# Performance work log

Measured on AMD Instinct MI355X. Metric: run time of the kernel, lower is better.

Reference implementation:

```python
import jax, jax.numpy as jnp
import numpy as np

EPS = 1e-12  # torch F.normalize default eps

def _l2norm(x, axis=-1):
    n = jnp.linalg.norm(x, axis=axis, keepdims=True)
    return x / jnp.maximum(n, EPS)

def setup_inputs() -> dict:
    key = jax.random.key(0)
    k1, k2 = jax.random.split(key)
    query = jax.random.normal(k1, (65536, 512), dtype=jnp.float32)
    prototypes = jax.random.normal(k2, (64, 512), dtype=jnp.float32)
    return {"query": query, "prototypes": prototypes, "k": 3}

def reference(query, prototypes, k):
    # cosine similarity between queries and prototypes: [B, P]
    sim = jnp.einsum('bd,pd->bp', _l2norm(query), _l2norm(prototypes))
    k = min(int(k), prototypes.shape[0])
    weights, indices = jax.lax.top_k(sim, k)          # [B, k]
    retrieved = prototypes[indices]                   # [B, k, D]
    w = jax.nn.softmax(weights, axis=1)               # [B, k]
    return jnp.einsum('bkd,bk->bd', retrieved, w)     # [B, D]
```

## Files before the change

### kernel.cpp

```cpp
#include <hip/hip_runtime.h>
#include <math.h>

#define DIM 512
#define NP  64
#define TAU 4e-5f
#define LISTCAP 8192
#define RFB 128

#define WS_PTW   0
#define WS_BHI   131072
#define WS_BLO   196608
#define WS_INV64 262144
#define WS_CNT   262656
#define WS_LIST  262784

typedef __attribute__((ext_vector_type(8))) short bf16x8;
typedef __attribute__((ext_vector_type(8))) unsigned short u16x8;
typedef __attribute__((ext_vector_type(4))) float f32x4;

__device__ __forceinline__ unsigned short f2bf(float f) {
  const unsigned int u = __float_as_uint(f);
  return (unsigned short)((u + 0x7FFFu + ((u >> 16) & 1u)) >> 16);
}
__device__ __forceinline__ float bf2f(unsigned short h) {
  return __uint_as_float(((unsigned int)h) << 16);
}

__device__ __forceinline__ void gload_lds16(const void* g, void* l) {
  __builtin_amdgcn_global_load_lds(
      (const __attribute__((address_space(1))) void*)g,
      (__attribute__((address_space(3))) void*)l, 16, 0, 0);
}

__device__ __forceinline__ void ins4f(float v, int idx, float& v0, float& v1,
                                      float& v2, float& v3, int& j0, int& j1,
                                      int& j2, int& j3) {
  const bool b0 = v > v0, b1 = v > v1, b2 = v > v2, b3 = v > v3;
  v3 = b2 ? v2 : (b3 ? v : v3);  j3 = b2 ? j2 : (b3 ? idx : j3);
  v2 = b1 ? v1 : (b2 ? v : v2);  j2 = b1 ? j1 : (b2 ? idx : j2);
  v1 = b0 ? v0 : (b1 ? v : v1);  j1 = b0 ? j0 : (b1 ? idx : j1);
  v0 = b0 ? v  : v0;             j0 = b0 ? idx : j0;
}

__device__ __forceinline__ void ins3d(double v, int idx, double& b0, double& b1,
                                      double& b2, int& k0, int& k1, int& k2) {
  const bool c0 = v > b0, c1 = v > b1, c2 = v > b2;
  b2 = c1 ? b1 : (c2 ? v : b2);  k2 = c1 ? k1 : (c2 ? idx : k2);
  b1 = c0 ? b0 : (c1 ? v : b1);  k1 = c0 ? k0 : (c1 ? idx : k1);
  b0 = c0 ? v  : b0;             k0 = c0 ? idx : k0;
}

__global__ __launch_bounds__(256) void prep_all_kernel(
    const float* __restrict__ protos, float* __restrict__ ptw,
    unsigned short* __restrict__ bhi, unsigned short* __restrict__ blo,
    double* __restrict__ inv64, int* __restrict__ cnt) {
  if (blockIdx.x == 0 && threadIdx.x == 0) *cnt = 0;
  const int p = blockIdx.x * 4 + (threadIdx.x >> 6);
  const int lane = threadIdx.x & 63;
  const float4* pr = (const float4*)(protos + (size_t)p * DIM);
  const float4 a = pr[lane * 2];
  const float4 b = pr[lane * 2 + 1];
  double ss = (double)a.x * a.x + (double)a.y * a.y + (double)a.z * a.z +
              (double)a.w * a.w + (double)b.x * b.x + (double)b.y * b.y +
              (double)b.z * b.z + (double)b.w * b.w;
#pragma unroll
  for (int m = 1; m < 64; m <<= 1) ss += __shfl_xor(ss, m);
  const double inv = 1.0 / fmax(sqrt(ss), 1e-12);
  if (lane == 0) inv64[p] = inv;
  const float v[8] = {a.x, a.y, a.z, a.w, b.x, b.y, b.z, b.w};
  u16x8 hi8, lo8;
#pragma unroll
  for (int e = 0; e < 8; ++e) {
    ptw[(size_t)(lane * 8 + e) * NP + p] = v[e];
    const float vh = (float)((double)v[e] * inv);
    const unsigned short h = f2bf(vh);
    hi8[e] = h;
    lo8[e] = f2bf(vh - bf2f(h));
  }
  const int ks = lane >> 2, lg = lane & 3, pt = p >> 4, lr = p & 15;
  const size_t base = ((size_t)(ks * 4 + pt) * 64 + lg * 16 + lr) * 8;
  *(u16x8*)&bhi[base] = hi8;
  *(u16x8*)&blo[base] = lo8;
}

__global__ __launch_bounds__(256) void sim_kernel(
    const float* __restrict__ query, const float* __restrict__ protos,
    const unsigned short* __restrict__ bhi_u, const unsigned short* __restrict__ blo_u,
    float* __restrict__ out, int* __restrict__ cnt, int* __restrict__ list) {
  __shared__ __align__(16) float Abuf[4][3][512];
  __shared__ float4 wiSw[4][16];

  const int t = threadIdx.x;
  const int wid = t >> 6;
  const int l = t & 63;
  const int lr = l & 15;
  const int lg = l >> 4;
  const int row0 = blockIdx.x * 64;
  const int wr0 = row0 + wid * 16;

  const int sgswz = ((l & 7) ^ (l >> 3)) << 4;
  const int srow = l >> 3;
  auto stage = [&](int cc) {
#pragma unroll
    for (int i = 0; i < 2; ++i) {
      const char* src = (const char*)query +
          (size_t)(wr0 + i * 8 + srow) * 2048 + cc * 128 + sgswz;
      gload_lds16(src, (char*)&Abuf[wid][cc % 3][0] + i * 1024);
    }
  };

  const bf16x8* bhp = (const bf16x8*)bhi_u;
  const bf16x8* blp = (const bf16x8*)blo_u;

  f32x4 acc[4] = {};
  float ss = 0.f;
  bf16x8 Bh[2][4], Bl[2][4];

  stage(0);
#pragma unroll
  for (int pt = 0; pt < 4; ++pt) {
    Bh[0][pt] = bhp[(size_t)(0 * 4 + pt) * 64 + l];
    Bl[0][pt] = blp[(size_t)(0 * 4 + pt) * 64 + l];
  }
  __builtin_amdgcn_sched_barrier(0);
  stage(1);
#pragma unroll
  for (int pt = 0; pt < 4; ++pt) {
    Bh[1][pt] = bhp[(size_t)(1 * 4 + pt) * 64 + l];
    Bl[1][pt] = blp[(size_t)(1 * 4 + pt) * 64 + l];
  }

  const int g0 = lg * 2;
  const int sw = lr & 7;
  const char* abase = (const char*)&Abuf[wid][0][0];

#define SIM_CHUNK(C, NV)                                                      \
  {                                                                           \
    asm volatile("s_waitcnt vmcnt(" #NV ")" ::: "memory");                    \
    __builtin_amdgcn_sched_barrier(0);                                        \
    if ((C) + 2 < 16) stage((C) + 2);                                         \
    const char* ab = abase + ((C) % 3) * 2048;                                \
    const float4 a0 = *(const float4*)(ab + lr * 128 + ((g0 ^ sw) << 4));     \
    const float4 a1 = *(const float4*)(ab + lr * 128 + (((g0 + 1) ^ sw) << 4)); \
    const float av[8] = {a0.x, a0.y, a0.z, a0.w, a1.x, a1.y, a1.z, a1.w};     \
    bf16x8 ahi, alo;                                                          \
    _Pragma("unroll")                                                         \
    for (int i = 0; i < 8; ++i) {                                             \
      const unsigned int u = __float_as_uint(av[i]);                          \
      const unsigned short h = (unsigned short)(u >> 16);                     \
      ahi[i] = (short)h;                                                      \
      alo[i] = (short)f2bf(av[i] - bf2f(h));                                  \
      ss += av[i] * av[i];                                                    \
    }                                                                         \
    const int bb = (C) & 1;                                                   \
    _Pragma("unroll")                                                         \
    for (int pt = 0; pt < 4; ++pt) {                                          \
      acc[pt] = __builtin_amdgcn_mfma_f32_16x16x32_bf16(ahi, Bh[bb][pt], acc[pt], 0, 0, 0); \
      acc[pt] = __builtin_amdgcn_mfma_f32_16x16x32_bf16(ahi, Bl[bb][pt], acc[pt], 0, 0, 0); \
      acc[pt] = __builtin_amdgcn_mfma_f32_16x16x32_bf16(alo, Bh[bb][pt], acc[pt], 0, 0, 0); \
    }                                                                         \
    if ((C) + 2 < 16) {                                                       \
      _Pragma("unroll")                                                       \
      for (int pt = 0; pt < 4; ++pt) {                                        \
        Bh[bb][pt] = bhp[(size_t)(((C) + 2) * 4 + pt) * 64 + l];              \
        Bl[bb][pt] = blp[(size_t)(((C) + 2) * 4 + pt) * 64 + l];              \
      }                                                                       \
    }                                                                         \
  }

  SIM_CHUNK(0, 10)  SIM_CHUNK(1, 10)  SIM_CHUNK(2, 10)  SIM_CHUNK(3, 10)
  SIM_CHUNK(4, 10)  SIM_CHUNK(5, 10)  SIM_CHUNK(6, 10)  SIM_CHUNK(7, 10)
  SIM_CHUNK(8, 10)  SIM_CHUNK(9, 10)  SIM_CHUNK(10, 10) SIM_CHUNK(11, 10)
  SIM_CHUNK(12, 10) SIM_CHUNK(13, 10) SIM_CHUNK(14, 10) SIM_CHUNK(15, 0)
#undef SIM_CHUNK

  ss += __shfl_xor(ss, 16);
  ss += __shfl_xor(ss, 32);

#pragma unroll
  for (int e = 0; e < 4; ++e) {
    float v0 = -1e30f, v1 = -1e30f, v2 = -1e30f, v3 = -1e30f;
    int j0 = 0, j1 = 0, j2 = 0, j3 = 0;
#pragma unroll
    for (int pt = 0; pt < 4; ++pt)
      ins4f(acc[pt][e], pt * 16 + lr, v0, v1, v2, v3, j0, j1, j2, j3);
#pragma unroll
    for (int m = 1; m <= 8; m <<= 1) {
      const float p0 = __shfl_xor(v0, m), p1 = __shfl_xor(v1, m);
      const float p2 = __shfl_xor(v2, m), p3 = __shfl_xor(v3, m);
      const int q0 = __shfl_xor(j0, m), q1 = __shfl_xor(j1, m);
      const int q2 = __shfl_xor(j2, m), q3 = __shfl_xor(j3, m);
      ins4f(p0, q0, v0, v1, v2, v3, j0, j1, j2, j3);
      ins4f(p1, q1, v0, v1, v2, v3, j0, j1, j2, j3);
      ins4f(p2, q2, v0, v1, v2, v3, j0, j1, j2, j3);
      ins4f(p3, q3, v0, v1, v2, v3, j0, j1, j2, j3);
    }
    const float ssr = __shfl(ss, lg * 4 + e);
    if (lr == 0) {
      const int row = lg * 4 + e;
      const float qi = 1.0f / fmaxf(sqrtf(ssr), 1e-12f);
      const float s0 = v0 * qi, s1 = v1 * qi, s2 = v2 * qi, s3 = v3 * qi;
      const float e1 = expf(s1 - s0), e2 = expf(s2 - s0);
      const float inv = 1.0f / (1.0f + e1 + e2);
      wiSw[wid][row] = make_float4(inv, e1 * inv, e2 * inv,
                                   __int_as_float(j0 | (j1 << 6) | (j2 << 12)));
      if (s2 - s3 < TAU) {
        const int pos = atomicAdd(cnt, 1);
        if (pos < LISTCAP) list[pos] = wr0 + row;
      }
    }
  }

#pragma unroll 2
  for (int r = 0; r < 16; ++r) {
    const float4 wi = wiSw[wid][r];
    const int pack = __float_as_int(wi.w);
    const int i0 = pack & 63, i1 = (pack >> 6) & 63, i2 = (pack >> 12) & 63;
    const float* p0 = protos + (size_t)i0 * DIM;
    const float* p1 = protos + (size_t)i1 * DIM;
    const float* p2 = protos + (size_t)i2 * DIM;
    float* orow = out + (size_t)(wr0 + r) * DIM;
#pragma unroll
    for (int h = 0; h < 2; ++h) {
      const int col = h * 256 + l * 4;
      const float4 x = *(const float4*)(p0 + col);
      const float4 y = *(const float4*)(p1 + col);
      const float4 z = *(const float4*)(p2 + col);
      float4 res;
      res.x = wi.x * x.x + wi.y * y.x + wi.z * z.x;
      res.y = wi.x * x.y + wi.y * y.y + wi.z * z.y;
      res.z = wi.x * x.z + wi.y * y.z + wi.z * z.z;
      res.w = wi.x * x.w + wi.y * y.w + wi.z * z.w;
      *(float4*)(orow + col) = res;
    }
  }
}

__global__ __launch_bounds__(256) void refine_kernel(
    const float* __restrict__ query, const float* __restrict__ protos,
    const float* __restrict__ ptw, const double* __restrict__ inv64,
    const int* __restrict__ cnt, const int* __restrict__ list,
    float* __restrict__ out) {
  const int n = min(*cnt, LISTCAP);
  const int lane = threadIdx.x & 63;
  const int gw = blockIdx.x * 4 + (threadIdx.x >> 6);

  for (int i = gw; i < n; i += RFB * 4) {
    const int row = list[i];
    const float* q = query + (size_t)row * DIM;
    double a0 = 0.0, a1 = 0.0, a2 = 0.0, a3 = 0.0;
    float qs = 0.f;
#pragma unroll 4
    for (int k = 0; k < DIM; k += 4) {
      const float4 qv = *(const float4*)(q + k);
      a0 = fma((double)qv.x, (double)ptw[(size_t)(k + 0) * NP + lane], a0);
      a1 = fma((double)qv.y, (double)ptw[(size_t)(k + 1) * NP + lane], a1);
      a2 = fma((double)qv.z, (double)ptw[(size_t)(k + 2) * NP + lane], a2);
      a3 = fma((double)qv.w, (double)ptw[(size_t)(k + 3) * NP + lane], a3);
      qs += qv.x * qv.x + qv.y * qv.y + qv.z * qv.z + qv.w * qv.w;
    }
    const double sim = (a0 + a1 + a2 + a3) * inv64[lane];

    double b0 = sim, b1 = -1e300, b2 = -1e300;
    int k0 = lane, k1 = 0, k2 = 0;
#pragma unroll
    for (int m = 1; m <= 32; m <<= 1) {
      const double p0 = __shfl_xor(b0, m), p1 = __shfl_xor(b1, m),
                   p2 = __shfl_xor(b2, m);
      const int q0 = __shfl_xor(k0, m), q1 = __shfl_xor(k1, m),
                q2 = __shfl_xor(k2, m);
      ins3d(p0, q0, b0, b1, b2, k0, k1, k2);
      ins3d(p1, q1, b0, b1, b2, k0, k1, k2);
      ins3d(p2, q2, b0, b1, b2, k0, k1, k2);
    }
    const double qi = 1.0 / fmax(sqrt((double)qs), 1e-12);
    const double s0 = b0 * qi, s1 = b1 * qi, s2 = b2 * qi;
    const double e1 = exp(s1 - s0), e2 = exp(s2 - s0);
    const double inv = 1.0 / (1.0 + e1 + e2);
    const double w0 = inv, w1 = e1 * inv, w2 = e2 * inv;
    const float* p0r = protos + (size_t)k0 * DIM;
    const float* p1r = protos + (size_t)k1 * DIM;
    const float* p2r = protos + (size_t)k2 * DIM;
#pragma unroll
    for (int u = 0; u < 2; ++u) {
      const int col = u * 256 + lane * 4;
      const float4 x = *(const float4*)(p0r + col);
      const float4 y = *(const float4*)(p1r + col);
      const float4 z = *(const float4*)(p2r + col);
      float4 res;
      res.x = (float)(w0 * x.x + w1 * y.x + w2 * z.x);
      res.y = (float)(w0 * x.y + w1 * y.y + w2 * z.y);
      res.z = (float)(w0 * x.z + w1 * y.z + w2 * z.z);
      res.w = (float)(w0 * x.w + w1 * y.w + w2 * z.w);
      *(float4*)(out + (size_t)row * DIM + col) = res;
    }
  }
}

extern "C" void kernel_launch(void* const* d_in, const int* in_sizes, int n_in,
                              void* d_out, int out_size, void* d_ws, size_t ws_size,
                              hipStream_t stream) {
  const float* query = (const float*)d_in[0];
  const float* protos = (const float*)d_in[1];
  float* out = (float*)d_out;
  float* ptw = (float*)((char*)d_ws + WS_PTW);
  unsigned short* bhi = (unsigned short*)((char*)d_ws + WS_BHI);
  unsigned short* blo = (unsigned short*)((char*)d_ws + WS_BLO);
  double* inv64 = (double*)((char*)d_ws + WS_INV64);
  int* cnt = (int*)((char*)d_ws + WS_CNT);
  int* list = (int*)((char*)d_ws + WS_LIST);

  const int nrows = in_sizes[0] / DIM;

  hipLaunchKernelGGL(prep_all_kernel, dim3(16), dim3(256), 0, stream,
                     protos, ptw, bhi, blo, inv64, cnt);
  hipLaunchKernelGGL(sim_kernel, dim3(nrows / 64), dim3(256), 0, stream,
                     query, protos, bhi, blo, out, cnt, list);
  hipLaunchKernelGGL(refine_kernel, dim3(RFB), dim3(256), 0, stream,
                     query, protos, ptw, inv64, cnt, list, out);
}
```

Measured before the change: 109.0 us.

## Drop bf16 low part of prototypes, widen refine threshold and list

Removes the hi/lo split of the normalized prototypes, so the similarity GEMM uses two bf16 MFMAs per tile instead of three and loads half the B fragments. The lower precision is compensated by raising the near-tie threshold TAU, which sends more rows to the exact refine pass, and by enlarging the list capacity and the refine grid to handle them. The tradeoff is less MFMA and load work in the main kernel against more rows re-examined in refine, with correctness depending on the new threshold bounding the added bf16 error.

```diff
diff --git a/kernel.cpp b/kernel.cpp
--- a/kernel.cpp
+++ b/kernel.cpp
@@ -3,16 +3,15 @@
 
 #define DIM 512
 #define NP  64
-#define TAU 4e-5f
-#define LISTCAP 8192
-#define RFB 128
+#define TAU 4.5e-4f
+#define LISTCAP 32768
+#define RFB 256
 
 #define WS_PTW   0
 #define WS_BHI   131072
-#define WS_BLO   196608
-#define WS_INV64 262144
-#define WS_CNT   262656
-#define WS_LIST  262784
+#define WS_INV64 196608
+#define WS_CNT   197120
+#define WS_LIST  197248
 
 typedef __attribute__((ext_vector_type(8))) short bf16x8;
 typedef __attribute__((ext_vector_type(8))) unsigned short u16x8;
@@ -52,8 +51,8 @@
 
 __global__ __launch_bounds__(256) void prep_all_kernel(
     const float* __restrict__ protos, float* __restrict__ ptw,
-    unsigned short* __restrict__ bhi, unsigned short* __restrict__ blo,
-    double* __restrict__ inv64, int* __restrict__ cnt) {
+    unsigned short* __restrict__ bhi, double* __restrict__ inv64,
+    int* __restrict__ cnt) {
   if (blockIdx.x == 0 && threadIdx.x == 0) *cnt = 0;
   const int p = blockIdx.x * 4 + (threadIdx.x >> 6);
   const int lane = threadIdx.x & 63;
@@ -68,24 +67,19 @@
   const double inv = 1.0 / fmax(sqrt(ss), 1e-12);
   if (lane == 0) inv64[p] = inv;
   const float v[8] = {a.x, a.y, a.z, a.w, b.x, b.y, b.z, b.w};
-  u16x8 hi8, lo8;
+  u16x8 hi8;
 #pragma unroll
   for (int e = 0; e < 8; ++e) {
     ptw[(size_t)(lane * 8 + e) * NP + p] = v[e];
-    const float vh = (float)((double)v[e] * inv);
-    const unsigned short h = f2bf(vh);
-    hi8[e] = h;
-    lo8[e] = f2bf(vh - bf2f(h));
+    hi8[e] = f2bf((float)((double)v[e] * inv));
   }
   const int ks = lane >> 2, lg = lane & 3, pt = p >> 4, lr = p & 15;
-  const size_t base = ((size_t)(ks * 4 + pt) * 64 + lg * 16 + lr) * 8;
-  *(u16x8*)&bhi[base] = hi8;
-  *(u16x8*)&blo[base] = lo8;
+  *(u16x8*)&bhi[((size_t)(ks * 4 + pt) * 64 + lg * 16 + lr) * 8] = hi8;
 }
 
 __global__ __launch_bounds__(256) void sim_kernel(
     const float* __restrict__ query, const float* __restrict__ protos,
-    const unsigned short* __restrict__ bhi_u, const unsigned short* __restrict__ blo_u,
+    const unsigned short* __restrict__ bhi_u,
     float* __restrict__ out, int* __restrict__ cnt, int* __restrict__ list) {
   __shared__ __align__(16) float Abuf[4][3][512];
   __shared__ float4 wiSw[4][16];
@@ -110,25 +104,18 @@
   };
 
   const bf16x8* bhp = (const bf16x8*)bhi_u;
-  const bf16x8* blp = (const bf16x8*)blo_u;
 
   f32x4 acc[4] = {};
   float ss = 0.f;
-  bf16x8 Bh[2][4], Bl[2][4];
+  bf16x8 Bh[2][4];
 
   stage(0);
 #pragma unroll
-  for (int pt = 0; pt < 4; ++pt) {
-    Bh[0][pt] = bhp[(size_t)(0 * 4 + pt) * 64 + l];
-    Bl[0][pt] = blp[(size_t)(0 * 4 + pt) * 64 + l];
-  }
+  for (int pt = 0; pt < 4; ++pt) Bh[0][pt] = bhp[(size_t)(0 * 4 + pt) * 64 + l];
   __builtin_amdgcn_sched_barrier(0);
   stage(1);
 #pragma unroll
-  for (int pt = 0; pt < 4; ++pt) {
-    Bh[1][pt] = bhp[(size_t)(1 * 4 + pt) * 64 + l];
-    Bl[1][pt] = blp[(size_t)(1 * 4 + pt) * 64 + l];
-  }
+  for (int pt = 0; pt < 4; ++pt) Bh[1][pt] = bhp[(size_t)(1 * 4 + pt) * 64 + l];
 
   const int g0 = lg * 2;
   const int sw = lr & 7;
@@ -156,22 +143,19 @@
     _Pragma("unroll")                                                         \
     for (int pt = 0; pt < 4; ++pt) {                                          \
       acc[pt] = __builtin_amdgcn_mfma_f32_16x16x32_bf16(ahi, Bh[bb][pt], acc[pt], 0, 0, 0); \
-      acc[pt] = __builtin_amdgcn_mfma_f32_16x16x32_bf16(ahi, Bl[bb][pt], acc[pt], 0, 0, 0); \
       acc[pt] = __builtin_amdgcn_mfma_f32_16x16x32_bf16(alo, Bh[bb][pt], acc[pt], 0, 0, 0); \
     }                                                                         \
     if ((C) + 2 < 16) {                                                       \
       _Pragma("unroll")                                                       \
-      for (int pt = 0; pt < 4; ++pt) {                                        \
+      for (int pt = 0; pt < 4; ++pt)                                          \
         Bh[bb][pt] = bhp[(size_t)(((C) + 2) * 4 + pt) * 64 + l];              \
-        Bl[bb][pt] = blp[(size_t)(((C) + 2) * 4 + pt) * 64 + l];              \
-      }                                                                       \
     }                                                                         \
   }
 
-  SIM_CHUNK(0, 10)  SIM_CHUNK(1, 10)  SIM_CHUNK(2, 10)  SIM_CHUNK(3, 10)
-  SIM_CHUNK(4, 10)  SIM_CHUNK(5, 10)  SIM_CHUNK(6, 10)  SIM_CHUNK(7, 10)
-  SIM_CHUNK(8, 10)  SIM_CHUNK(9, 10)  SIM_CHUNK(10, 10) SIM_CHUNK(11, 10)
-  SIM_CHUNK(12, 10) SIM_CHUNK(13, 10) SIM_CHUNK(14, 10) SIM_CHUNK(15, 0)
+  SIM_CHUNK(0, 6)   SIM_CHUNK(1, 6)   SIM_CHUNK(2, 6)   SIM_CHUNK(3, 6)
+  SIM_CHUNK(4, 6)   SIM_CHUNK(5, 6)   SIM_CHUNK(6, 6)   SIM_CHUNK(7, 6)
+  SIM_CHUNK(8, 6)   SIM_CHUNK(9, 6)   SIM_CHUNK(10, 6)  SIM_CHUNK(11, 6)
+  SIM_CHUNK(12, 6)  SIM_CHUNK(13, 6)  SIM_CHUNK(14, 6)  SIM_CHUNK(15, 0)
 #undef SIM_CHUNK
 
   ss += __shfl_xor(ss, 16);
@@ -305,7 +289,6 @@
   float* out = (float*)d_out;
   float* ptw = (float*)((char*)d_ws + WS_PTW);
   unsigned short* bhi = (unsigned short*)((char*)d_ws + WS_BHI);
-  unsigned short* blo = (unsigned short*)((char*)d_ws + WS_BLO);
   double* inv64 = (double*)((char*)d_ws + WS_INV64);
   int* cnt = (int*)((char*)d_ws + WS_CNT);
   int* list = (int*)((char*)d_ws + WS_LIST);
@@ -313,9 +296,9 @@
   const int nrows = in_sizes[0] / DIM;
 
   hipLaunchKernelGGL(prep_all_kernel, dim3(16), dim3(256), 0, stream,
-                     protos, ptw, bhi, blo, inv64, cnt);
+                     protos, ptw, bhi, inv64, cnt);
   hipLaunchKernelGGL(sim_kernel, dim3(nrows / 64), dim3(256), 0, stream,
-                     query, protos, bhi, blo, out, cnt, list);
+                     query, protos, bhi, out, cnt, list);
   hipLaunchKernelGGL(refine_kernel, dim3(RFB), dim3(256), 0, stream,
                      query, protos, ptw, inv64, cnt, list, out);
 }
```

New measurement: 164.9 us. +51.3%, slower.

## Split prototype columns across wave pairs and merge top-k through LDS

Applied to the files above, without the earlier changes.

Doubles the block to 512 threads so each 16-row group is handled by two waves, each computing similarity against half of the 64 prototypes. This halves the per-wave MFMA work and register footprint and adds more waves in flight to hide latency. The per-half top-4 lists are merged through shared memory before the softmax and the near-tie flagging. The output write is spread across all eight waves. In exchange, both waves of a pair stage the same query rows into their own LDS buffers, which doubles query load traffic, and the kernel adds two block-wide barriers.

```diff
diff --git a/kernel.cpp b/kernel.cpp
--- a/kernel.cpp
+++ b/kernel.cpp
@@ -83,20 +83,24 @@
   *(u16x8*)&blo[base] = lo8;
 }
 
-__global__ __launch_bounds__(256) void sim_kernel(
+__global__ __launch_bounds__(512) void sim_kernel(
     const float* __restrict__ query, const float* __restrict__ protos,
     const unsigned short* __restrict__ bhi_u, const unsigned short* __restrict__ blo_u,
     float* __restrict__ out, int* __restrict__ cnt, int* __restrict__ list) {
-  __shared__ __align__(16) float Abuf[4][3][512];
-  __shared__ float4 wiSw[4][16];
+  __shared__ __align__(16) float Abuf[8][3][512];
+  __shared__ float4 topV[8][16];
+  __shared__ int4   topJ[8][16];
+  __shared__ float4 wiS[64];
 
   const int t = threadIdx.x;
-  const int wid = t >> 6;
+  const int w = t >> 6;
   const int l = t & 63;
+  const int pr_ = w >> 1;
+  const int h = w & 1;
   const int lr = l & 15;
   const int lg = l >> 4;
   const int row0 = blockIdx.x * 64;
-  const int wr0 = row0 + wid * 16;
+  const int wr0 = row0 + pr_ * 16;
 
   const int sgswz = ((l & 7) ^ (l >> 3)) << 4;
   const int srow = l >> 3;
@@ -105,34 +109,34 @@
     for (int i = 0; i < 2; ++i) {
       const char* src = (const char*)query +
           (size_t)(wr0 + i * 8 + srow) * 2048 + cc * 128 + sgswz;
-      gload_lds16(src, (char*)&Abuf[wid][cc % 3][0] + i * 1024);
+      gload_lds16(src, (char*)&Abuf[w][cc % 3][0] + i * 1024);
     }
   };
 
   const bf16x8* bhp = (const bf16x8*)bhi_u;
   const bf16x8* blp = (const bf16x8*)blo_u;
 
-  f32x4 acc[4] = {};
+  f32x4 acc[2] = {};
   float ss = 0.f;
-  bf16x8 Bh[2][4], Bl[2][4];
+  bf16x8 Bh[2][2], Bl[2][2];
 
   stage(0);
 #pragma unroll
-  for (int pt = 0; pt < 4; ++pt) {
-    Bh[0][pt] = bhp[(size_t)(0 * 4 + pt) * 64 + l];
-    Bl[0][pt] = blp[(size_t)(0 * 4 + pt) * 64 + l];
+  for (int pt = 0; pt < 2; ++pt) {
+    Bh[0][pt] = bhp[(size_t)(0 * 4 + 2 * h + pt) * 64 + l];
+    Bl[0][pt] = blp[(size_t)(0 * 4 + 2 * h + pt) * 64 + l];
   }
   __builtin_amdgcn_sched_barrier(0);
   stage(1);
 #pragma unroll
-  for (int pt = 0; pt < 4; ++pt) {
-    Bh[1][pt] = bhp[(size_t)(1 * 4 + pt) * 64 + l];
-    Bl[1][pt] = blp[(size_t)(1 * 4 + pt) * 64 + l];
+  for (int pt = 0; pt < 2; ++pt) {
+    Bh[1][pt] = bhp[(size_t)(1 * 4 + 2 * h + pt) * 64 + l];
+    Bl[1][pt] = blp[(size_t)(1 * 4 + 2 * h + pt) * 64 + l];
   }
 
   const int g0 = lg * 2;
   const int sw = lr & 7;
-  const char* abase = (const char*)&Abuf[wid][0][0];
+  const char* abase = (const char*)&Abuf[w][0][0];
 
 #define SIM_CHUNK(C, NV)                                                      \
   {                                                                           \
@@ -147,31 +151,31 @@
     _Pragma("unroll")                                                         \
     for (int i = 0; i < 8; ++i) {                                             \
       const unsigned int u = __float_as_uint(av[i]);                          \
-      const unsigned short h = (unsigned short)(u >> 16);                     \
-      ahi[i] = (short)h;                                                      \
-      alo[i] = (short)f2bf(av[i] - bf2f(h));                                  \
+      const unsigned short hh = (unsigned short)(u >> 16);                    \
+      ahi[i] = (short)hh;                                                     \
+      alo[i] = (short)f2bf(av[i] - bf2f(hh));                                 \
       ss += av[i] * av[i];                                                    \
     }                                                                         \
     const int bb = (C) & 1;                                                   \
     _Pragma("unroll")                                                         \
-    for (int pt = 0; pt < 4; ++pt) {                                          \
+    for (int pt = 0; pt < 2; ++pt) {                                          \
       acc[pt] = __builtin_amdgcn_mfma_f32_16x16x32_bf16(ahi, Bh[bb][pt], acc[pt], 0, 0, 0); \
       acc[pt] = __builtin_amdgcn_mfma_f32_16x16x32_bf16(ahi, Bl[bb][pt], acc[pt], 0, 0, 0); \
       acc[pt] = __builtin_amdgcn_mfma_f32_16x16x32_bf16(alo, Bh[bb][pt], acc[pt], 0, 0, 0); \
     }                                                                         \
     if ((C) + 2 < 16) {                                                       \
       _Pragma("unroll")                                                       \
-      for (int pt = 0; pt < 4; ++pt) {                                        \
-        Bh[bb][pt] = bhp[(size_t)(((C) + 2) * 4 + pt) * 64 + l];              \
-        Bl[bb][pt] = blp[(size_t)(((C) + 2) * 4 + pt) * 64 + l];              \
+      for (int pt = 0; pt < 2; ++pt) {                                        \
+        Bh[bb][pt] = bhp[(size_t)(((C) + 2) * 4 + 2 * h + pt) * 64 + l];      \
+        Bl[bb][pt] = blp[(size_t)(((C) + 2) * 4 + 2 * h + pt) * 64 + l];      \
       }                                                                       \
     }                                                                         \
   }
 
-  SIM_CHUNK(0, 10)  SIM_CHUNK(1, 10)  SIM_CHUNK(2, 10)  SIM_CHUNK(3, 10)
-  SIM_CHUNK(4, 10)  SIM_CHUNK(5, 10)  SIM_CHUNK(6, 10)  SIM_CHUNK(7, 10)
-  SIM_CHUNK(8, 10)  SIM_CHUNK(9, 10)  SIM_CHUNK(10, 10) SIM_CHUNK(11, 10)
-  SIM_CHUNK(12, 10) SIM_CHUNK(13, 10) SIM_CHUNK(14, 10) SIM_CHUNK(15, 0)
+  SIM_CHUNK(0, 6)   SIM_CHUNK(1, 6)   SIM_CHUNK(2, 6)   SIM_CHUNK(3, 6)
+  SIM_CHUNK(4, 6)   SIM_CHUNK(5, 6)   SIM_CHUNK(6, 6)   SIM_CHUNK(7, 6)
+  SIM_CHUNK(8, 6)   SIM_CHUNK(9, 6)   SIM_CHUNK(10, 6)  SIM_CHUNK(11, 6)
+  SIM_CHUNK(12, 6)  SIM_CHUNK(13, 6)  SIM_CHUNK(14, 6)  SIM_CHUNK(15, 0)
 #undef SIM_CHUNK
 
   ss += __shfl_xor(ss, 16);
@@ -181,9 +185,8 @@
   for (int e = 0; e < 4; ++e) {
     float v0 = -1e30f, v1 = -1e30f, v2 = -1e30f, v3 = -1e30f;
     int j0 = 0, j1 = 0, j2 = 0, j3 = 0;
-#pragma unroll
-    for (int pt = 0; pt < 4; ++pt)
-      ins4f(acc[pt][e], pt * 16 + lr, v0, v1, v2, v3, j0, j1, j2, j3);
+    ins4f(acc[0][e], (2 * h + 0) * 16 + lr, v0, v1, v2, v3, j0, j1, j2, j3);
+    ins4f(acc[1][e], (2 * h + 1) * 16 + lr, v0, v1, v2, v3, j0, j1, j2, j3);
 #pragma unroll
     for (int m = 1; m <= 8; m <<= 1) {
       const float p0 = __shfl_xor(v0, m), p1 = __shfl_xor(v1, m);
@@ -195,34 +198,53 @@
       ins4f(p2, q2, v0, v1, v2, v3, j0, j1, j2, j3);
       ins4f(p3, q3, v0, v1, v2, v3, j0, j1, j2, j3);
     }
-    const float ssr = __shfl(ss, lg * 4 + e);
     if (lr == 0) {
-      const int row = lg * 4 + e;
-      const float qi = 1.0f / fmaxf(sqrtf(ssr), 1e-12f);
-      const float s0 = v0 * qi, s1 = v1 * qi, s2 = v2 * qi, s3 = v3 * qi;
-      const float e1 = expf(s1 - s0), e2 = expf(s2 - s0);
-      const float inv = 1.0f / (1.0f + e1 + e2);
-      wiSw[wid][row] = make_float4(inv, e1 * inv, e2 * inv,
-                                   __int_as_float(j0 | (j1 << 6) | (j2 << 12)));
-      if (s2 - s3 < TAU) {
-        const int pos = atomicAdd(cnt, 1);
-        if (pos < LISTCAP) list[pos] = wr0 + row;
-      }
-    }
-  }
+      const int r = lg * 4 + e;
+      topV[w][r] = make_float4(v0, v1, v2, v3);
+      topJ[w][r] = make_int4(j0, j1, j2, j3);
+    }
+  }
+  __syncthreads();
+
+  if (h == 0 && l < 16) {
+    const int r = l;
+    float v0 = -1e30f, v1 = -1e30f, v2 = -1e30f, v3 = -1e30f;
+    int j0 = 0, j1 = 0, j2 = 0, j3 = 0;
+#pragma unroll
+    for (int m = 0; m < 2; ++m) {
+      const float4 tv = topV[w + m][r];
+      const int4 tj = topJ[w + m][r];
+      ins4f(tv.x, tj.x, v0, v1, v2, v3, j0, j1, j2, j3);
+      ins4f(tv.y, tj.y, v0, v1, v2, v3, j0, j1, j2, j3);
+      ins4f(tv.z, tj.z, v0, v1, v2, v3, j0, j1, j2, j3);
+      ins4f(tv.w, tj.w, v0, v1, v2, v3, j0, j1, j2, j3);
+    }
+    const float qi = 1.0f / fmaxf(sqrtf(ss), 1e-12f);
+    const float s0 = v0 * qi, s1 = v1 * qi, s2 = v2 * qi, s3 = v3 * qi;
+    const float e1 = expf(s1 - s0), e2 = expf(s2 - s0);
+    const float inv = 1.0f / (1.0f + e1 + e2);
+    wiS[pr_ * 16 + r] = make_float4(inv, e1 * inv, e2 * inv,
+                                    __int_as_float(j0 | (j1 << 6) | (j2 << 12)));
+    if (s2 - s3 < TAU) {
+      const int pos = atomicAdd(cnt, 1);
+      if (pos < LISTCAP) list[pos] = wr0 + r;
+    }
+  }
+  __syncthreads();
 
 #pragma unroll 2
-  for (int r = 0; r < 16; ++r) {
-    const float4 wi = wiSw[wid][r];
+  for (int r = 0; r < 8; ++r) {
+    const int row = w * 8 + r;
+    const float4 wi = wiS[row];
     const int pack = __float_as_int(wi.w);
     const int i0 = pack & 63, i1 = (pack >> 6) & 63, i2 = (pack >> 12) & 63;
     const float* p0 = protos + (size_t)i0 * DIM;
     const float* p1 = protos + (size_t)i1 * DIM;
     const float* p2 = protos + (size_t)i2 * DIM;
-    float* orow = out + (size_t)(wr0 + r) * DIM;
-#pragma unroll
-    for (int h = 0; h < 2; ++h) {
-      const int col = h * 256 + l * 4;
+    float* orow = out + (size_t)(row0 + row) * DIM;
+#pragma unroll
+    for (int hh = 0; hh < 2; ++hh) {
+      const int col = hh * 256 + l * 4;
       const float4 x = *(const float4*)(p0 + col);
       const float4 y = *(const float4*)(p1 + col);
       const float4 z = *(const float4*)(p2 + col);
@@ -314,7 +336,7 @@
 
   hipLaunchKernelGGL(prep_all_kernel, dim3(16), dim3(256), 0, stream,
                      protos, ptw, bhi, blo, inv64, cnt);
-  hipLaunchKernelGGL(sim_kernel, dim3(nrows / 64), dim3(256), 0, stream,
+  hipLaunchKernelGGL(sim_kernel, dim3(nrows / 64), dim3(512), 0, stream,
                      query, protos, bhi, blo, out, cnt, list);
   hipLaunchKernelGGL(refine_kernel, dim3(RFB), dim3(256), 0, stream,
                      query, protos, ptw, inv64, cnt, list, out);
```

After: 140.4 us. +28.8%, slower.
